# Kernel tuning notes

Hardware: AMD Instinct MI355X
Metric: run time of the kernel (lower is better)

Reference implementation:

```python
import jax, jax.numpy as jnp
import numpy as np

BSZ, P, D, C = 16, 4096, 256, 512


def setup_inputs() -> dict:
    key = jax.random.key(0)
    k1, k2 = jax.random.split(key)
    x = jax.random.normal(k1, (BSZ, P, D), dtype=jnp.float32)
    kernels = jax.random.normal(k2, (C, D), dtype=jnp.float32) * 0.001
    return {"x": x, "kernels": kernels}


def reference(x, kernels):
    bsz, Pn, d = x.shape
    # (bsz, P, C) projection scores, ReLU'd
    scores = jax.nn.relu(jnp.einsum('bpd,cd->bpc', x, kernels))
    # per-channel argmax over positions -> (bsz, C)
    idx = jnp.argmax(scores, axis=1)
    # scatter_add each kernel row into its winning position
    b_idx = jnp.arange(bsz)[:, None]  # (bsz, 1) broadcast against (bsz, C)
    src = jnp.broadcast_to(kernels, (bsz,) + kernels.shape)  # (bsz, C, d)
    out = jnp.zeros((bsz, Pn, d), dtype=x.dtype).at[b_idx, idx].add(src)
    return out
```

## Files before the change

kernel.cpp:

```cpp
#include <hip/hip_runtime.h>
#include <cstddef>
#include <cstdint>

#define BSZ 16
#define PN  4096
#define DD  256
#define CC  512
#define TP  128
#define TC  128
#define NPT (PN / TP)
#define NKC 8

typedef short bf16x8 __attribute__((ext_vector_type(8)));
typedef float f32x4  __attribute__((ext_vector_type(4)));

#define MEMFENCE() __asm__ __volatile__("" ::: "memory")
#define WAITCNT_VM8 0x1F78
#define WAITCNT_VM0 0x1F70

struct Top2 { float v1, v2; int i1, i2; };

__device__ __forceinline__ void t2_insert(Top2& t, float v, int i) {
  if (v > t.v1 || (v == t.v1 && i < t.i1)) {
    t.v2 = t.v1; t.i2 = t.i1; t.v1 = v; t.i1 = i;
  } else if (v > t.v2 || (v == t.v2 && i < t.i2)) {
    t.v2 = v; t.i2 = i;
  }
}

__device__ __forceinline__ void split4(float4 v, uint2& hp, uint2& lp) {
  uint32_t u0 = __float_as_uint(v.x), u1 = __float_as_uint(v.y),
           u2 = __float_as_uint(v.z), u3 = __float_as_uint(v.w);
  float l0 = v.x - __uint_as_float(u0 & 0xffff0000u);
  float l1 = v.y - __uint_as_float(u1 & 0xffff0000u);
  float l2 = v.z - __uint_as_float(u2 & 0xffff0000u);
  float l3 = v.w - __uint_as_float(u3 & 0xffff0000u);
  hp.x = __builtin_amdgcn_perm(u1, u0, 0x07060302u);
  hp.y = __builtin_amdgcn_perm(u3, u2, 0x07060302u);
  lp.x = __builtin_amdgcn_perm(__float_as_uint(l1), __float_as_uint(l0), 0x07060302u);
  lp.y = __builtin_amdgcn_perm(__float_as_uint(l3), __float_as_uint(l2), 0x07060302u);
}

__device__ __forceinline__ void gld16(const void* gsrc, void* ldst) {
  __builtin_amdgcn_global_load_lds(
      (const __attribute__((address_space(1))) unsigned int*)gsrc,
      (__attribute__((address_space(3))) unsigned int*)ldst, 16, 0, 0);
}

__global__ __launch_bounds__(256) void convert_k_kernel(
    const float* __restrict__ kern, uint32_t* __restrict__ ks) {
  const int kc = blockIdx.x, ct = blockIdx.y;
  const size_t chunk = ((size_t)ct * NKC + kc) * 4096;
#pragma unroll
  for (int s0 = 0; s0 < 2; s0++) {
    int s  = threadIdx.x + s0 * 256;
    int fp = s >> 6, kg = (s >> 4) & 3, lr = s & 15;
    int r  = fp * 16 + lr, k0 = kg * 8;
    const float* src = kern + ((size_t)ct * TC + r) * DD + kc * 32 + k0;
    float4 v0 = *(const float4*)src, v1 = *(const float4*)(src + 4);
    uint2 h0, l0, h1, l1; split4(v0, h0, l0); split4(v1, h1, l1);
    *(uint4*)&ks[chunk + (size_t)s * 4]        = make_uint4(h0.x, h0.y, h1.x, h1.y);
    *(uint4*)&ks[chunk + 2048 + (size_t)s * 4] = make_uint4(l0.x, l0.y, l1.x, l1.y);
  }
}

__global__ __launch_bounds__(256) void score_kernel(
    const float* __restrict__ x, const uint32_t* __restrict__ ks,
    float2* __restrict__ pv2, uint32_t* __restrict__ pix) {

  __shared__ __align__(16) char lds[65536];

  const int ct = blockIdx.x, pt = blockIdx.y, b = blockIdx.z;
  const int tid  = threadIdx.x;
  const int lane = tid & 63, wave = tid >> 6;
  const int wr = wave >> 1, wc = wave & 1;

  const char* xbase = (const char*)(x + ((size_t)b * PN + (size_t)pt * TP) * DD);
  const char* asrc[4];
#pragma unroll
  for (int i = 0; i < 4; i++) {
    int s = i * 256 + tid;
    int swr = s >> 9, sfp = (s >> 7) & 3, sl = (s >> 1) & 63, sh = s & 1;
    int row = swr * 64 + sfp * 16 + (sl & 15);
    asrc[i] = xbase + (size_t)row * (DD * 4) + (sl >> 4) * 32 + sh * 16;
  }
  const char* bsrc = (const char*)ks + ((size_t)ct * NKC) * 16384 + tid * 16;

  f32x4 acc[4][4];
#pragma unroll
  for (int i = 0; i < 4; i++)
#pragma unroll
    for (int j = 0; j < 4; j++) acc[i][j] = (f32x4)0.f;

  auto issue = [&](int kc) {
    char* Ab = lds + (kc & 1) * 16384;
    char* Bb = lds + 32768 + (kc & 1) * 16384;
#pragma unroll
    for (int i = 0; i < 4; i++)
      gld16(asrc[i] + kc * 128, Ab + i * 4096 + tid * 16);
#pragma unroll
    for (int i = 0; i < 4; i++)
      gld16(bsrc + kc * 16384 + i * 4096, Bb + i * 4096 + tid * 16);
  };

  issue(0);
  for (int kc = 0; kc < NKC; kc++) {
    if (kc + 1 < NKC) issue(kc + 1);
    MEMFENCE();
    if (kc + 1 < NKC) {
      __builtin_amdgcn_s_waitcnt(WAITCNT_VM8);
    } else {
      __builtin_amdgcn_s_waitcnt(WAITCNT_VM0);
    }
    __builtin_amdgcn_s_barrier();
    MEMFENCE();

    const char* Ab = lds + (kc & 1) * 16384;
    const char* Bb = lds + 32768 + (kc & 1) * 16384;

    bf16x8 Ah[4], Al[4];
#pragma unroll
    for (int fp = 0; fp < 4; fp++) {
      const float4* ap = (const float4*)(Ab + wr * 8192 + fp * 2048 + lane * 32);
      float4 v0 = ap[0], v1 = ap[1];
      uint2 h0, l0, h1, l1; split4(v0, h0, l0); split4(v1, h1, l1);
      uint4 hh = make_uint4(h0.x, h0.y, h1.x, h1.y);
      uint4 ll = make_uint4(l0.x, l0.y, l1.x, l1.y);
      Ah[fp] = *(bf16x8*)&hh;
      Al[fp] = *(bf16x8*)&ll;
    }
#pragma unroll
    for (int fc = 0; fc < 4; fc++) {
      const char* bp = Bb + wc * 4096 + fc * 1024 + lane * 16;
      bf16x8 Bh = *(const bf16x8*)bp;
      bf16x8 Bl = *(const bf16x8*)(bp + 8192);
#pragma unroll
      for (int fp = 0; fp < 4; fp++) {
        acc[fp][fc] = __builtin_amdgcn_mfma_f32_16x16x32_bf16(Ah[fp], Bh, acc[fp][fc], 0, 0, 0);
        acc[fp][fc] = __builtin_amdgcn_mfma_f32_16x16x32_bf16(Ah[fp], Bl, acc[fp][fc], 0, 0, 0);
        acc[fp][fc] = __builtin_amdgcn_mfma_f32_16x16x32_bf16(Al[fp], Bh, acc[fp][fc], 0, 0, 0);
      }
    }
    MEMFENCE();
    __builtin_amdgcn_s_barrier();
    MEMFENCE();
  }
  __syncthreads();

  const int lr = lane & 15, kg = lane >> 4;
  float4* scratch = (float4*)lds;
  const int slot = wr * 4 + kg;
#pragma unroll
  for (int fc = 0; fc < 4; fc++) {
    Top2 t; t.v1 = -1.f; t.v2 = -1.f; t.i1 = 0x7fffffff; t.i2 = 0x7fffffff;
#pragma unroll
    for (int fp = 0; fp < 4; fp++)
#pragma unroll
      for (int r = 0; r < 4; r++) {
        float v = acc[fp][fc][r]; v = v > 0.f ? v : 0.f;
        t2_insert(t, v, wr * 64 + fp * 16 + kg * 4 + r);
      }
    int c_local = wc * 64 + fc * 16 + lr;
    scratch[slot * TC + c_local] =
        make_float4(t.v1, __int_as_float(t.i1), t.v2, __int_as_float(t.i2));
  }
  __syncthreads();

  if (tid < TC) {
    Top2 t; t.v1 = -1.f; t.v2 = -1.f; t.i1 = 0x7fffffff; t.i2 = 0x7fffffff;
#pragma unroll
    for (int s = 0; s < 8; s++) {
      float4 e = scratch[s * TC + tid];
      t2_insert(t, e.x, __float_as_int(e.y));
      t2_insert(t, e.z, __float_as_int(e.w));
    }
    int c = ct * TC + tid;
    size_t o = ((size_t)b * CC + c) * NPT + pt;
    uint32_t p1 = (uint32_t)(pt * TP + t.i1);
    uint32_t p2 = (uint32_t)(pt * TP + t.i2);
    pv2[o] = make_float2(t.v1, t.v2);
    pix[o] = (p1 << 16) | (p2 & 0xffffu);
  }
}

__global__ __launch_bounds__(64) void reduce_winner_kernel(
    const float2* __restrict__ pv2, const uint32_t* __restrict__ pix,
    const float* __restrict__ x, const float* __restrict__ kern,
    int* __restrict__ winner) {
  const int c = blockIdx.x, b = blockIdx.y;
  const int l = threadIdx.x;

  Top2 t; t.v1 = -1.f; t.v2 = -1.f; t.i1 = 0x7fffffff; t.i2 = 0x7fffffff;
  if (l < NPT) {
    size_t o = ((size_t)b * CC + c) * NPT + l;
    float2 v = pv2[o]; uint32_t ii = pix[o];
    t.v1 = v.x; t.v2 = v.y; t.i1 = (int)(ii >> 16); t.i2 = (int)(ii & 0xffffu);
  }
#pragma unroll
  for (int m = 1; m < 64; m <<= 1) {
    float uv1 = __shfl_xor(t.v1, m, 64);
    int   ui1 = __shfl_xor(t.i1, m, 64);
    float uv2 = __shfl_xor(t.v2, m, 64);
    int   ui2 = __shfl_xor(t.i2, m, 64);
    t2_insert(t, uv1, ui1);
    t2_insert(t, uv2, ui2);
  }

  int win = t.i1;
  if (t.v1 - t.v2 <= 1e-4f * t.v1 + 1e-5f) {
    const float4* x1 = (const float4*)(x + ((size_t)b * PN + t.i1) * DD);
    const float4* x2 = (const float4*)(x + ((size_t)b * PN + t.i2) * DD);
    const float4* kc = (const float4*)(kern + (size_t)c * DD);
    float4 a1 = x1[l], a2 = x2[l], k4 = kc[l];
    float s1 = a1.x * k4.x + a1.y * k4.y + a1.z * k4.z + a1.w * k4.w;
    float s2 = a2.x * k4.x + a2.y * k4.y + a2.z * k4.z + a2.w * k4.w;
#pragma unroll
    for (int m = 1; m < 64; m <<= 1) {
      s1 += __shfl_xor(s1, m, 64);
      s2 += __shfl_xor(s2, m, 64);
    }
    s1 = fmaxf(s1, 0.f); s2 = fmaxf(s2, 0.f);
    if (s2 > s1 || (s2 == s1 && t.i2 < t.i1)) win = t.i2;
  }
  if (l == 0) winner[(size_t)b * CC + c] = win;
}

__global__ __launch_bounds__(256) void write_out_kernel(
    const int* __restrict__ winner, const float* __restrict__ kern,
    float4* __restrict__ out) {
  __shared__ __align__(16) int wrow[CC];
  const int b = blockIdx.y;
  const int tid = threadIdx.x, lane = tid & 63, w = tid >> 6;
  const int p = blockIdx.x * 4 + w;

  *(int2*)&wrow[tid * 2] = *(const int2*)&winner[(size_t)b * CC + tid * 2];
  __syncthreads();

  int4 w0 = *(const int4*)&wrow[lane * 8];
  int4 w1 = *(const int4*)&wrow[lane * 8 + 4];
  int wv[8] = {w0.x, w0.y, w0.z, w0.w, w1.x, w1.y, w1.z, w1.w};

  float4 acc = make_float4(0.f, 0.f, 0.f, 0.f);
#pragma unroll
  for (int j = 0; j < 8; j++) {
    unsigned long long m = __ballot(wv[j] == p);
    while (m) {
      int bit = __ffsll((long long)m) - 1; m &= m - 1;
      int c = bit * 8 + j;
      float4 kv = ((const float4*)(kern + (size_t)c * DD))[lane];
      acc.x += kv.x; acc.y += kv.y; acc.z += kv.z; acc.w += kv.w;
    }
  }
  out[((size_t)b * PN + p) * 64 + lane] = acc;
}

extern "C" void kernel_launch(void* const* d_in, const int* in_sizes, int n_in,
                              void* d_out, int out_size, void* d_ws, size_t ws_size,
                              hipStream_t stream) {
  const float* x    = (const float*)d_in[0];
  const float* kern = (const float*)d_in[1];
  float* out = (float*)d_out;

  char* ws = (char*)d_ws;
  float2*   pv2 = (float2*)ws;
  uint32_t* pix = (uint32_t*)(ws + (size_t)BSZ * CC * NPT * sizeof(float2));
  uint32_t* ks  = (uint32_t*)(ws + 3u * 1024 * 1024);
  int*      win = (int*)(ws + 3u * 1024 * 1024 + 512u * 1024);

  convert_k_kernel<<<dim3(NKC, CC / TC), 256, 0, stream>>>(kern, ks);

  score_kernel<<<dim3(CC / TC, NPT, BSZ), 256, 0, stream>>>(x, ks, pv2, pix);

  reduce_winner_kernel<<<dim3(CC, BSZ), 64, 0, stream>>>(pv2, pix, x, kern, win);

  write_out_kernel<<<dim3(PN / 4, BSZ), 256, 0, stream>>>(win, kern, (float4*)out);
}
```

Before: 199.4 us.

## Load score operands directly to registers, remap block order, batch reduce and write kernels

The score kernel drops the LDS double-buffered global_load_lds pipeline. Each wave now loads its x rows and pre-split kernel fragments straight from global memory into registers, with register prefetch of the next k-chunk, and uses occupancy hint 2. The grid is flattened to 1D with a swizzled mapping so the four channel tiles of the same x tile run close together for L2 reuse. The reduce kernel packs four channels per 256-thread block, and the write-out kernel handles four positions per wave. The change removes barriers and LDS traffic but gives up sharing loads across waves, so x and B are fetched redundantly per wave through cache.

```diff
diff --git a/kernel.cpp b/kernel.cpp
--- a/kernel.cpp
+++ b/kernel.cpp
@@ -13,10 +13,6 @@
 
 typedef short bf16x8 __attribute__((ext_vector_type(8)));
 typedef float f32x4  __attribute__((ext_vector_type(4)));
-
-#define MEMFENCE() __asm__ __volatile__("" ::: "memory")
-#define WAITCNT_VM8 0x1F78
-#define WAITCNT_VM0 0x1F70
 
 struct Top2 { float v1, v2; int i1, i2; };
 
@@ -41,12 +37,6 @@
   lp.y = __builtin_amdgcn_perm(__float_as_uint(l3), __float_as_uint(l2), 0x07060302u);
 }
 
-__device__ __forceinline__ void gld16(const void* gsrc, void* ldst) {
-  __builtin_amdgcn_global_load_lds(
-      (const __attribute__((address_space(1))) unsigned int*)gsrc,
-      (__attribute__((address_space(3))) unsigned int*)ldst, 16, 0, 0);
-}
-
 __global__ __launch_bounds__(256) void convert_k_kernel(
     const float* __restrict__ kern, uint32_t* __restrict__ ks) {
   const int kc = blockIdx.x, ct = blockIdx.y;
@@ -64,27 +54,27 @@
   }
 }
 
-__global__ __launch_bounds__(256) void score_kernel(
+__global__ __launch_bounds__(256, 2) void score_kernel(
     const float* __restrict__ x, const uint32_t* __restrict__ ks,
     float2* __restrict__ pv2, uint32_t* __restrict__ pix) {
 
-  __shared__ __align__(16) char lds[65536];
-
-  const int ct = blockIdx.x, pt = blockIdx.y, b = blockIdx.z;
+  __shared__ __align__(16) float4 scratch[8 * TC];
+
+  const int id = blockIdx.x;
+  const int ct = (id >> 3) & 3;
+  const int pb = ((id >> 5) << 3) | (id & 7);
+  const int pt = pb & 31;
+  const int b  = pb >> 5;
+
   const int tid  = threadIdx.x;
   const int lane = tid & 63, wave = tid >> 6;
   const int wr = wave >> 1, wc = wave & 1;
-
-  const char* xbase = (const char*)(x + ((size_t)b * PN + (size_t)pt * TP) * DD);
-  const char* asrc[4];
-#pragma unroll
-  for (int i = 0; i < 4; i++) {
-    int s = i * 256 + tid;
-    int swr = s >> 9, sfp = (s >> 7) & 3, sl = (s >> 1) & 63, sh = s & 1;
-    int row = swr * 64 + sfp * 16 + (sl & 15);
-    asrc[i] = xbase + (size_t)row * (DD * 4) + (sl >> 4) * 32 + sh * 16;
-  }
-  const char* bsrc = (const char*)ks + ((size_t)ct * NKC) * 16384 + tid * 16;
+  const int lr = lane & 15, kg = lane >> 4;
+
+  const char* abase = (const char*)x
+      + (size_t)(b * PN + pt * TP + wr * 64 + lr) * (DD * 4) + kg * 32;
+  const char* bbase = (const char*)ks + (size_t)ct * NKC * 16384
+      + wc * 4096 + lane * 16;
 
   f32x4 acc[4][4];
 #pragma unroll
@@ -92,63 +82,53 @@
 #pragma unroll
     for (int j = 0; j < 4; j++) acc[i][j] = (f32x4)0.f;
 
-  auto issue = [&](int kc) {
-    char* Ab = lds + (kc & 1) * 16384;
-    char* Bb = lds + 32768 + (kc & 1) * 16384;
-#pragma unroll
-    for (int i = 0; i < 4; i++)
-      gld16(asrc[i] + kc * 128, Ab + i * 4096 + tid * 16);
-#pragma unroll
-    for (int i = 0; i < 4; i++)
-      gld16(bsrc + kc * 16384 + i * 4096, Bb + i * 4096 + tid * 16);
-  };
-
-  issue(0);
+  float4 a_cur[4][2], a_nxt[4][2];
+#pragma unroll
+  for (int fp = 0; fp < 4; fp++) {
+    a_cur[fp][0] = *(const float4*)(abase + fp * 16384);
+    a_cur[fp][1] = *(const float4*)(abase + fp * 16384 + 16);
+  }
+
   for (int kc = 0; kc < NKC; kc++) {
-    if (kc + 1 < NKC) issue(kc + 1);
-    MEMFENCE();
     if (kc + 1 < NKC) {
-      __builtin_amdgcn_s_waitcnt(WAITCNT_VM8);
-    } else {
-      __builtin_amdgcn_s_waitcnt(WAITCNT_VM0);
-    }
-    __builtin_amdgcn_s_barrier();
-    MEMFENCE();
-
-    const char* Ab = lds + (kc & 1) * 16384;
-    const char* Bb = lds + 32768 + (kc & 1) * 16384;
-
+#pragma unroll
+      for (int fp = 0; fp < 4; fp++) {
+        a_nxt[fp][0] = *(const float4*)(abase + fp * 16384 + (kc + 1) * 128);
+        a_nxt[fp][1] = *(const float4*)(abase + fp * 16384 + (kc + 1) * 128 + 16);
+      }
+    }
+    bf16x8 Bh[4], Bl[4];
+#pragma unroll
+    for (int fc = 0; fc < 4; fc++) {
+      Bh[fc] = *(const bf16x8*)(bbase + kc * 16384 + fc * 1024);
+      Bl[fc] = *(const bf16x8*)(bbase + kc * 16384 + fc * 1024 + 8192);
+    }
     bf16x8 Ah[4], Al[4];
 #pragma unroll
     for (int fp = 0; fp < 4; fp++) {
-      const float4* ap = (const float4*)(Ab + wr * 8192 + fp * 2048 + lane * 32);
-      float4 v0 = ap[0], v1 = ap[1];
-      uint2 h0, l0, h1, l1; split4(v0, h0, l0); split4(v1, h1, l1);
+      uint2 h0, l0, h1, l1;
+      split4(a_cur[fp][0], h0, l0);
+      split4(a_cur[fp][1], h1, l1);
       uint4 hh = make_uint4(h0.x, h0.y, h1.x, h1.y);
       uint4 ll = make_uint4(l0.x, l0.y, l1.x, l1.y);
       Ah[fp] = *(bf16x8*)&hh;
       Al[fp] = *(bf16x8*)&ll;
     }
 #pragma unroll
-    for (int fc = 0; fc < 4; fc++) {
-      const char* bp = Bb + wc * 4096 + fc * 1024 + lane * 16;
-      bf16x8 Bh = *(const bf16x8*)bp;
-      bf16x8 Bl = *(const bf16x8*)(bp + 8192);
+    for (int fc = 0; fc < 4; fc++)
 #pragma unroll
       for (int fp = 0; fp < 4; fp++) {
-        acc[fp][fc] = __builtin_amdgcn_mfma_f32_16x16x32_bf16(Ah[fp], Bh, acc[fp][fc], 0, 0, 0);
-        acc[fp][fc] = __builtin_amdgcn_mfma_f32_16x16x32_bf16(Ah[fp], Bl, acc[fp][fc], 0, 0, 0);
-        acc[fp][fc] = __builtin_amdgcn_mfma_f32_16x16x32_bf16(Al[fp], Bh, acc[fp][fc], 0, 0, 0);
-      }
-    }
-    MEMFENCE();
-    __builtin_amdgcn_s_barrier();
-    MEMFENCE();
-  }
-  __syncthreads();
-
-  const int lr = lane & 15, kg = lane >> 4;
-  float4* scratch = (float4*)lds;
+        acc[fp][fc] = __builtin_amdgcn_mfma_f32_16x16x32_bf16(Ah[fp], Bh[fc], acc[fp][fc], 0, 0, 0);
+        acc[fp][fc] = __builtin_amdgcn_mfma_f32_16x16x32_bf16(Ah[fp], Bl[fc], acc[fp][fc], 0, 0, 0);
+        acc[fp][fc] = __builtin_amdgcn_mfma_f32_16x16x32_bf16(Al[fp], Bh[fc], acc[fp][fc], 0, 0, 0);
+      }
+#pragma unroll
+    for (int fp = 0; fp < 4; fp++) {
+      a_cur[fp][0] = a_nxt[fp][0];
+      a_cur[fp][1] = a_nxt[fp][1];
+    }
+  }
+
   const int slot = wr * 4 + kg;
 #pragma unroll
   for (int fc = 0; fc < 4; fc++) {
@@ -183,12 +163,13 @@
   }
 }
 
-__global__ __launch_bounds__(64) void reduce_winner_kernel(
+__global__ __launch_bounds__(256) void reduce_winner_kernel(
     const float2* __restrict__ pv2, const uint32_t* __restrict__ pix,
     const float* __restrict__ x, const float* __restrict__ kern,
     int* __restrict__ winner) {
-  const int c = blockIdx.x, b = blockIdx.y;
-  const int l = threadIdx.x;
+  const int c = blockIdx.x * 4 + (threadIdx.x >> 6);
+  const int b = blockIdx.y;
+  const int l = threadIdx.x & 63;
 
   Top2 t; t.v1 = -1.f; t.v2 = -1.f; t.i1 = 0x7fffffff; t.i2 = 0x7fffffff;
   if (l < NPT) {
@@ -231,7 +212,6 @@
   __shared__ __align__(16) int wrow[CC];
   const int b = blockIdx.y;
   const int tid = threadIdx.x, lane = tid & 63, w = tid >> 6;
-  const int p = blockIdx.x * 4 + w;
 
   *(int2*)&wrow[tid * 2] = *(const int2*)&winner[(size_t)b * CC + tid * 2];
   __syncthreads();
@@ -240,18 +220,22 @@
   int4 w1 = *(const int4*)&wrow[lane * 8 + 4];
   int wv[8] = {w0.x, w0.y, w0.z, w0.w, w1.x, w1.y, w1.z, w1.w};
 
-  float4 acc = make_float4(0.f, 0.f, 0.f, 0.f);
-#pragma unroll
-  for (int j = 0; j < 8; j++) {
-    unsigned long long m = __ballot(wv[j] == p);
-    while (m) {
-      int bit = __ffsll((long long)m) - 1; m &= m - 1;
-      int c = bit * 8 + j;
-      float4 kv = ((const float4*)(kern + (size_t)c * DD))[lane];
-      acc.x += kv.x; acc.y += kv.y; acc.z += kv.z; acc.w += kv.w;
-    }
-  }
-  out[((size_t)b * PN + p) * 64 + lane] = acc;
+#pragma unroll
+  for (int pi = 0; pi < 4; pi++) {
+    const int p = blockIdx.x * 16 + w * 4 + pi;
+    float4 acc = make_float4(0.f, 0.f, 0.f, 0.f);
+#pragma unroll
+    for (int j = 0; j < 8; j++) {
+      unsigned long long m = __ballot(wv[j] == p);
+      while (m) {
+        int bit = __ffsll((long long)m) - 1; m &= m - 1;
+        int c = bit * 8 + j;
+        float4 kv = ((const float4*)(kern + (size_t)c * DD))[lane];
+        acc.x += kv.x; acc.y += kv.y; acc.z += kv.z; acc.w += kv.w;
+      }
+    }
+    out[((size_t)b * PN + p) * 64 + lane] = acc;
+  }
 }
 
 extern "C" void kernel_launch(void* const* d_in, const int* in_sizes, int n_in,
@@ -269,9 +253,9 @@
 
   convert_k_kernel<<<dim3(NKC, CC / TC), 256, 0, stream>>>(kern, ks);
 
-  score_kernel<<<dim3(CC / TC, NPT, BSZ), 256, 0, stream>>>(x, ks, pv2, pix);
-
-  reduce_winner_kernel<<<dim3(CC, BSZ), 64, 0, stream>>>(pv2, pix, x, kern, win);
-
-  write_out_kernel<<<dim3(PN / 4, BSZ), 256, 0, stream>>>(win, kern, (float4*)out);
-}
+  score_kernel<<<dim3(4 * NPT * BSZ), 256, 0, stream>>>(x, ks, pv2, pix);
+
+  reduce_winner_kernel<<<dim3(CC / 4, BSZ), 256, 0, stream>>>(pv2, pix, x, kern, win);
+
+  write_out_kernel<<<dim3(PN / 16, BSZ), 256, 0, stream>>>(win, kern, (float4*)out);
+}
```

Result: slower. 225.0 us (+12.9%).

## Switch scoring to scaled fp16 two-term MFMA and fuse winner reduction into score kernel

Applied to the files above, without the earlier changes.

The bf16 three-term split becomes a two-term scheme: x goes to fp16 directly and the kernels are scaled and split into fp16 hi/lo, cutting MFMA count per tile from three to two. A last-block atomic counter folds the per-channel reduction into the score kernel, removing one launch. Near-ties within a fixed band are re-checked with double-precision dot products, which may rescan whole position tiles. The LDS double buffer is replaced by single buffering with syncthreads, and write_out handles four positions per wave. Together these trade pipelining and exactness margin for fewer matrix instructions and launches, and depend on the fixed band covering the fp16 error.

```diff
diff --git a/kernel.cpp b/kernel.cpp
--- a/kernel.cpp
+++ b/kernel.cpp
@@ -1,4 +1,5 @@
 #include <hip/hip_runtime.h>
+#include <hip/hip_fp16.h>
 #include <cstddef>
 #include <cstdint>
 
@@ -10,13 +11,11 @@
 #define TC  128
 #define NPT (PN / TP)
 #define NKC 8
-
-typedef short bf16x8 __attribute__((ext_vector_type(8)));
-typedef float f32x4  __attribute__((ext_vector_type(4)));
-
-#define MEMFENCE() __asm__ __volatile__("" ::: "memory")
-#define WAITCNT_VM8 0x1F78
-#define WAITCNT_VM0 0x1F70
+#define KSCALE 1024.0f
+#define BAND 0.15f
+
+typedef _Float16 f16x8 __attribute__((ext_vector_type(8)));
+typedef float    f32x4 __attribute__((ext_vector_type(4)));
 
 struct Top2 { float v1, v2; int i1, i2; };
 
@@ -28,17 +27,13 @@
   }
 }
 
-__device__ __forceinline__ void split4(float4 v, uint2& hp, uint2& lp) {
-  uint32_t u0 = __float_as_uint(v.x), u1 = __float_as_uint(v.y),
-           u2 = __float_as_uint(v.z), u3 = __float_as_uint(v.w);
-  float l0 = v.x - __uint_as_float(u0 & 0xffff0000u);
-  float l1 = v.y - __uint_as_float(u1 & 0xffff0000u);
-  float l2 = v.z - __uint_as_float(u2 & 0xffff0000u);
-  float l3 = v.w - __uint_as_float(u3 & 0xffff0000u);
-  hp.x = __builtin_amdgcn_perm(u1, u0, 0x07060302u);
-  hp.y = __builtin_amdgcn_perm(u3, u2, 0x07060302u);
-  lp.x = __builtin_amdgcn_perm(__float_as_uint(l1), __float_as_uint(l0), 0x07060302u);
-  lp.y = __builtin_amdgcn_perm(__float_as_uint(l3), __float_as_uint(l2), 0x07060302u);
+__device__ __forceinline__ f16x8 cvt8(float4 a, float4 b) {
+  f16x8 r;
+  r[0] = (_Float16)a.x; r[1] = (_Float16)a.y;
+  r[2] = (_Float16)a.z; r[3] = (_Float16)a.w;
+  r[4] = (_Float16)b.x; r[5] = (_Float16)b.y;
+  r[6] = (_Float16)b.z; r[7] = (_Float16)b.w;
+  return r;
 }
 
 __device__ __forceinline__ void gld16(const void* gsrc, void* ldst) {
@@ -47,9 +42,23 @@
       (__attribute__((address_space(3))) unsigned int*)ldst, 16, 0, 0);
 }
 
+__device__ __forceinline__ double dot64(const float* __restrict__ xr,
+                                        const float* __restrict__ kr, int lane) {
+  int o = lane * 4;
+  double s = (double)xr[o] * (double)kr[o]
+           + (double)xr[o + 1] * (double)kr[o + 1]
+           + (double)xr[o + 2] * (double)kr[o + 2]
+           + (double)xr[o + 3] * (double)kr[o + 3];
+#pragma unroll
+  for (int m = 1; m < 64; m <<= 1) s += __shfl_xor(s, m, 64);
+  return s;
+}
+
 __global__ __launch_bounds__(256) void convert_k_kernel(
-    const float* __restrict__ kern, uint32_t* __restrict__ ks) {
+    const float* __restrict__ kern, uint32_t* __restrict__ ks,
+    int* __restrict__ cnt) {
   const int kc = blockIdx.x, ct = blockIdx.y;
+  if (kc == 0 && ct == 0 && threadIdx.x < 64) cnt[threadIdx.x] = 0;
   const size_t chunk = ((size_t)ct * NKC + kc) * 4096;
 #pragma unroll
   for (int s0 = 0; s0 < 2; s0++) {
@@ -58,29 +67,42 @@
     int r  = fp * 16 + lr, k0 = kg * 8;
     const float* src = kern + ((size_t)ct * TC + r) * DD + kc * 32 + k0;
     float4 v0 = *(const float4*)src, v1 = *(const float4*)(src + 4);
-    uint2 h0, l0, h1, l1; split4(v0, h0, l0); split4(v1, h1, l1);
-    *(uint4*)&ks[chunk + (size_t)s * 4]        = make_uint4(h0.x, h0.y, h1.x, h1.y);
-    *(uint4*)&ks[chunk + 2048 + (size_t)s * 4] = make_uint4(l0.x, l0.y, l1.x, l1.y);
+    float sv[8] = {v0.x, v0.y, v0.z, v0.w, v1.x, v1.y, v1.z, v1.w};
+    f16x8 hi, lo;
+#pragma unroll
+    for (int i = 0; i < 8; i++) {
+      float sc = sv[i] * KSCALE;
+      _Float16 h = (_Float16)sc;
+      hi[i] = h;
+      lo[i] = (_Float16)(sc - (float)h);
+    }
+    *(uint4*)&ks[chunk + (size_t)s * 4]        = *(uint4*)&hi;
+    *(uint4*)&ks[chunk + 2048 + (size_t)s * 4] = *(uint4*)&lo;
   }
 }
 
 __global__ __launch_bounds__(256) void score_kernel(
     const float* __restrict__ x, const uint32_t* __restrict__ ks,
-    float2* __restrict__ pv2, uint32_t* __restrict__ pix) {
-
-  __shared__ __align__(16) char lds[65536];
+    const float* __restrict__ kern,
+    float2* __restrict__ pv2, uint32_t* __restrict__ pix,
+    int* __restrict__ win, int* __restrict__ cnt) {
+
+  __shared__ __align__(16) char lds[32768];
+  __shared__ int lastflag, nf;
+  __shared__ short flist[TC];
 
   const int ct = blockIdx.x, pt = blockIdx.y, b = blockIdx.z;
   const int tid  = threadIdx.x;
   const int lane = tid & 63, wave = tid >> 6;
   const int wr = wave >> 1, wc = wave & 1;
-
-  const char* xbase = (const char*)(x + ((size_t)b * PN + (size_t)pt * TP) * DD);
+  const int lr = lane & 15, kg = lane >> 4;
+
+  const char* xbase = (const char*)x + ((size_t)b * PN + (size_t)pt * TP) * (DD * 4);
   const char* asrc[4];
 #pragma unroll
   for (int i = 0; i < 4; i++) {
     int s = i * 256 + tid;
-    int swr = s >> 9, sfp = (s >> 7) & 3, sl = (s >> 1) & 63, sh = s & 1;
+    int swr = s >> 9, sfp = (s >> 7) & 3, sh = (s >> 6) & 1, sl = s & 63;
     int row = swr * 64 + sfp * 16 + (sl & 15);
     asrc[i] = xbase + (size_t)row * (DD * 4) + (sl >> 4) * 32 + sh * 16;
   }
@@ -92,62 +114,37 @@
 #pragma unroll
     for (int j = 0; j < 4; j++) acc[i][j] = (f32x4)0.f;
 
-  auto issue = [&](int kc) {
-    char* Ab = lds + (kc & 1) * 16384;
-    char* Bb = lds + 32768 + (kc & 1) * 16384;
+  for (int kc = 0; kc < NKC; kc++) {
 #pragma unroll
     for (int i = 0; i < 4; i++)
-      gld16(asrc[i] + kc * 128, Ab + i * 4096 + tid * 16);
+      gld16(asrc[i] + kc * 128, lds + i * 4096 + tid * 16);
 #pragma unroll
     for (int i = 0; i < 4; i++)
-      gld16(bsrc + kc * 16384 + i * 4096, Bb + i * 4096 + tid * 16);
-  };
-
-  issue(0);
-  for (int kc = 0; kc < NKC; kc++) {
-    if (kc + 1 < NKC) issue(kc + 1);
-    MEMFENCE();
-    if (kc + 1 < NKC) {
-      __builtin_amdgcn_s_waitcnt(WAITCNT_VM8);
-    } else {
-      __builtin_amdgcn_s_waitcnt(WAITCNT_VM0);
-    }
-    __builtin_amdgcn_s_barrier();
-    MEMFENCE();
-
-    const char* Ab = lds + (kc & 1) * 16384;
-    const char* Bb = lds + 32768 + (kc & 1) * 16384;
-
-    bf16x8 Ah[4], Al[4];
+      gld16(bsrc + kc * 16384 + i * 4096, lds + 16384 + i * 4096 + tid * 16);
+    __syncthreads();
+
+    f16x8 Ah[4];
 #pragma unroll
     for (int fp = 0; fp < 4; fp++) {
-      const float4* ap = (const float4*)(Ab + wr * 8192 + fp * 2048 + lane * 32);
-      float4 v0 = ap[0], v1 = ap[1];
-      uint2 h0, l0, h1, l1; split4(v0, h0, l0); split4(v1, h1, l1);
-      uint4 hh = make_uint4(h0.x, h0.y, h1.x, h1.y);
-      uint4 ll = make_uint4(l0.x, l0.y, l1.x, l1.y);
-      Ah[fp] = *(bf16x8*)&hh;
-      Al[fp] = *(bf16x8*)&ll;
+      const char* apb = lds + wr * 8192 + fp * 2048 + lane * 16;
+      float4 r0 = *(const float4*)apb;
+      float4 r1 = *(const float4*)(apb + 1024);
+      Ah[fp] = cvt8(r0, r1);
     }
 #pragma unroll
     for (int fc = 0; fc < 4; fc++) {
-      const char* bp = Bb + wc * 4096 + fc * 1024 + lane * 16;
-      bf16x8 Bh = *(const bf16x8*)bp;
-      bf16x8 Bl = *(const bf16x8*)(bp + 8192);
+      const char* bp = lds + 16384 + wc * 4096 + fc * 1024 + lane * 16;
+      f16x8 Bh = *(const f16x8*)bp;
+      f16x8 Bl = *(const f16x8*)(bp + 8192);
 #pragma unroll
       for (int fp = 0; fp < 4; fp++) {
-        acc[fp][fc] = __builtin_amdgcn_mfma_f32_16x16x32_bf16(Ah[fp], Bh, acc[fp][fc], 0, 0, 0);
-        acc[fp][fc] = __builtin_amdgcn_mfma_f32_16x16x32_bf16(Ah[fp], Bl, acc[fp][fc], 0, 0, 0);
-        acc[fp][fc] = __builtin_amdgcn_mfma_f32_16x16x32_bf16(Al[fp], Bh, acc[fp][fc], 0, 0, 0);
-      }
-    }
-    MEMFENCE();
-    __builtin_amdgcn_s_barrier();
-    MEMFENCE();
-  }
-  __syncthreads();
-
-  const int lr = lane & 15, kg = lane >> 4;
+        acc[fp][fc] = __builtin_amdgcn_mfma_f32_16x16x32_f16(Ah[fp], Bh, acc[fp][fc], 0, 0, 0);
+        acc[fp][fc] = __builtin_amdgcn_mfma_f32_16x16x32_f16(Ah[fp], Bl, acc[fp][fc], 0, 0, 0);
+      }
+    }
+    __syncthreads();
+  }
+
   float4* scratch = (float4*)lds;
   const int slot = wr * 4 + kg;
 #pragma unroll
@@ -181,48 +178,90 @@
     pv2[o] = make_float2(t.v1, t.v2);
     pix[o] = (p1 << 16) | (p2 & 0xffffu);
   }
-}
-
-__global__ __launch_bounds__(64) void reduce_winner_kernel(
-    const float2* __restrict__ pv2, const uint32_t* __restrict__ pix,
-    const float* __restrict__ x, const float* __restrict__ kern,
-    int* __restrict__ winner) {
-  const int c = blockIdx.x, b = blockIdx.y;
-  const int l = threadIdx.x;
-
-  Top2 t; t.v1 = -1.f; t.v2 = -1.f; t.i1 = 0x7fffffff; t.i2 = 0x7fffffff;
-  if (l < NPT) {
-    size_t o = ((size_t)b * CC + c) * NPT + l;
-    float2 v = pv2[o]; uint32_t ii = pix[o];
-    t.v1 = v.x; t.v2 = v.y; t.i1 = (int)(ii >> 16); t.i2 = (int)(ii & 0xffffu);
-  }
-#pragma unroll
-  for (int m = 1; m < 64; m <<= 1) {
-    float uv1 = __shfl_xor(t.v1, m, 64);
-    int   ui1 = __shfl_xor(t.i1, m, 64);
-    float uv2 = __shfl_xor(t.v2, m, 64);
-    int   ui2 = __shfl_xor(t.i2, m, 64);
-    t2_insert(t, uv1, ui1);
-    t2_insert(t, uv2, ui2);
-  }
-
-  int win = t.i1;
-  if (t.v1 - t.v2 <= 1e-4f * t.v1 + 1e-5f) {
-    const float4* x1 = (const float4*)(x + ((size_t)b * PN + t.i1) * DD);
-    const float4* x2 = (const float4*)(x + ((size_t)b * PN + t.i2) * DD);
-    const float4* kc = (const float4*)(kern + (size_t)c * DD);
-    float4 a1 = x1[l], a2 = x2[l], k4 = kc[l];
-    float s1 = a1.x * k4.x + a1.y * k4.y + a1.z * k4.z + a1.w * k4.w;
-    float s2 = a2.x * k4.x + a2.y * k4.y + a2.z * k4.z + a2.w * k4.w;
-#pragma unroll
-    for (int m = 1; m < 64; m <<= 1) {
-      s1 += __shfl_xor(s1, m, 64);
-      s2 += __shfl_xor(s2, m, 64);
-    }
-    s1 = fmaxf(s1, 0.f); s2 = fmaxf(s2, 0.f);
-    if (s2 > s1 || (s2 == s1 && t.i2 < t.i1)) win = t.i2;
-  }
-  if (l == 0) winner[(size_t)b * CC + c] = win;
+
+  __threadfence();
+  if (tid == 0) lastflag = (atomicAdd(&cnt[b * 4 + ct], 1) == NPT - 1);
+  __syncthreads();
+  if (!lastflag) return;
+  __threadfence();
+  if (tid == 0) nf = 0;
+  __syncthreads();
+
+  if (tid < TC) {
+    int c = ct * TC + tid;
+    size_t base = ((size_t)b * CC + c) * NPT;
+    Top2 g; g.v1 = -1.f; g.v2 = -1.f; g.i1 = 0x7fffffff; g.i2 = 0x7fffffff;
+    for (int i = 0; i < NPT; i++) {
+      float2 v = pv2[base + i]; uint32_t ii = pix[base + i];
+      t2_insert(g, v.x, (int)(ii >> 16));
+      t2_insert(g, v.y, (int)(ii & 0xffffu));
+    }
+    if (g.v1 - g.v2 > BAND) {
+      win[b * CC + c] = g.i1;
+    } else {
+      int idx = atomicAdd(&nf, 1);
+      flist[idx] = (short)tid;
+    }
+  }
+  __syncthreads();
+
+  for (int f = wave; f < nf; f += 4) {
+    int c = ct * TC + flist[f];
+    size_t base = ((size_t)b * CC + c) * NPT;
+    float v1t = -1.f, v2t = -1.f; int i1t = 0, i2t = 0;
+    if (lane < NPT) {
+      float2 v = pv2[base + lane]; uint32_t ii = pix[base + lane];
+      v1t = v.x; v2t = v.y; i1t = (int)(ii >> 16); i2t = (int)(ii & 0xffffu);
+    }
+    float gv = v1t;
+#pragma unroll
+    for (int m = 1; m < 64; m <<= 1) gv = fmaxf(gv, __shfl_xor(gv, m, 64));
+    float thr = gv - BAND;
+    unsigned long long m1 = __ballot(lane < NPT && v1t >= thr);
+    unsigned long long m2 = __ballot(lane < NPT && v2t >= thr);
+
+    const float* xb = x + (size_t)b * PN * DD;
+    const float* kr = kern + (size_t)c * DD;
+    double bv = 0.0; int bp_ = 0;
+
+    unsigned long long mm = m1;
+    while (mm) {
+      int sl_ = __ffsll((long long)mm) - 1; mm &= mm - 1;
+      int p = __shfl(i1t, sl_, 64);
+      double s = dot64(xb + (size_t)p * DD, kr, lane);
+      if (s > bv || (s == bv && p < bp_)) { bv = s; bp_ = p; }
+    }
+    mm = m2;
+    while (mm) {
+      int sl_ = __ffsll((long long)mm) - 1; mm &= mm - 1;
+      int p = __shfl(i2t, sl_, 64);
+      double s = dot64(xb + (size_t)p * DD, kr, lane);
+      if (s > bv || (s == bv && p < bp_)) { bv = s; bp_ = p; }
+    }
+    mm = m2;
+    while (mm) {
+      int tl = __ffsll((long long)mm) - 1; mm &= mm - 1;
+      const float* xA = xb + (size_t)(tl * TP + lane) * DD;
+      const float* xB = xA + (size_t)64 * DD;
+      double sA = 0.0, sB = 0.0;
+      for (int i = 0; i < DD; i++) {
+        double kv = (double)kr[i];
+        sA += (double)xA[i] * kv;
+        sB += (double)xB[i] * kv;
+      }
+      double lv = sA; int lp = tl * TP + lane;
+      if (sB > lv) { lv = sB; lp = tl * TP + lane + 64; }
+#pragma unroll
+      for (int m = 1; m < 64; m <<= 1) {
+        double ov = __shfl_xor(lv, m, 64);
+        int    op = __shfl_xor(lp, m, 64);
+        if (ov > lv || (ov == lv && op < lp)) { lv = ov; lp = op; }
+      }
+      if (lv > bv || (lv == bv && lp < bp_)) { bv = lv; bp_ = lp; }
+    }
+    if (bv <= 0.0) bp_ = 0;
+    if (lane == 0) win[b * CC + c] = bp_;
+  }
 }
 
 __global__ __launch_bounds__(256) void write_out_kernel(
@@ -231,27 +270,30 @@
   __shared__ __align__(16) int wrow[CC];
   const int b = blockIdx.y;
   const int tid = threadIdx.x, lane = tid & 63, w = tid >> 6;
-  const int p = blockIdx.x * 4 + w;
 
   *(int2*)&wrow[tid * 2] = *(const int2*)&winner[(size_t)b * CC + tid * 2];
   __syncthreads();
 
-  int4 w0 = *(const int4*)&wrow[lane * 8];
-  int4 w1 = *(const int4*)&wrow[lane * 8 + 4];
-  int wv[8] = {w0.x, w0.y, w0.z, w0.w, w1.x, w1.y, w1.z, w1.w};
-
-  float4 acc = make_float4(0.f, 0.f, 0.f, 0.f);
-#pragma unroll
-  for (int j = 0; j < 8; j++) {
-    unsigned long long m = __ballot(wv[j] == p);
-    while (m) {
-      int bit = __ffsll((long long)m) - 1; m &= m - 1;
-      int c = bit * 8 + j;
-      float4 kv = ((const float4*)(kern + (size_t)c * DD))[lane];
-      acc.x += kv.x; acc.y += kv.y; acc.z += kv.z; acc.w += kv.w;
-    }
-  }
-  out[((size_t)b * PN + p) * 64 + lane] = acc;
+  int wv[8];
+#pragma unroll
+  for (int j = 0; j < 8; j++) wv[j] = wrow[j * 64 + lane];
+
+#pragma unroll
+  for (int pi = 0; pi < 4; pi++) {
+    const int p = blockIdx.x * 16 + w * 4 + pi;
+    float4 acc = make_float4(0.f, 0.f, 0.f, 0.f);
+#pragma unroll
+    for (int j = 0; j < 8; j++) {
+      unsigned long long m = __ballot(wv[j] == p);
+      while (m) {
+        int bit = __ffsll((long long)m) - 1; m &= m - 1;
+        int c = j * 64 + bit;
+        float4 kv = ((const float4*)(kern + (size_t)c * DD))[lane];
+        acc.x += kv.x; acc.y += kv.y; acc.z += kv.z; acc.w += kv.w;
+      }
+    }
+    out[((size_t)b * PN + p) * 64 + lane] = acc;
+  }
 }
 
 extern "C" void kernel_launch(void* const* d_in, const int* in_sizes, int n_in,
@@ -266,12 +308,12 @@
   uint32_t* pix = (uint32_t*)(ws + (size_t)BSZ * CC * NPT * sizeof(float2));
   uint32_t* ks  = (uint32_t*)(ws + 3u * 1024 * 1024);
   int*      win = (int*)(ws + 3u * 1024 * 1024 + 512u * 1024);
-
-  convert_k_kernel<<<dim3(NKC, CC / TC), 256, 0, stream>>>(kern, ks);
-
-  score_kernel<<<dim3(CC / TC, NPT, BSZ), 256, 0, stream>>>(x, ks, pv2, pix);
-
-  reduce_winner_kernel<<<dim3(CC, BSZ), 64, 0, stream>>>(pv2, pix, x, kern, win);
-
-  write_out_kernel<<<dim3(PN / 4, BSZ), 256, 0, stream>>>(win, kern, (float4*)out);
-}
+  int*      cnt = (int*)(ws + 3u * 1024 * 1024 + 512u * 1024 + 32u * 1024);
+
+  convert_k_kernel<<<dim3(NKC, CC / TC), 256, 0, stream>>>(kern, ks, cnt);
+
+  score_kernel<<<dim3(CC / TC, NPT, BSZ), 256, 0, stream>>>(
+      x, ks, kern, pv2, pix, win, cnt);
+
+  write_out_kernel<<<dim3(PN / 16, BSZ), 256, 0, stream>>>(win, kern, (float4*)out);
+}
```

Measured after the change: 439.7 us. +120.5%, slower.
